# Kernel optimization log

Hardware: AMD Instinct MI355X
Metric: run time of the kernel (lower is better)

## Reference

```python
import jax, jax.numpy as jnp
import numpy as np

B, S, D = 2, 4096, 512
H, DQK, DV, W = 8, 64, 64, 32
ORDER = 6  # 2^(2*6)=4096 cells: 64x64 Hilbert grid covers max_seq_len=4096


def hilbert_d2xy(d, order):
    """Vectorized standard Hilbert curve d->(x,y) mapping on a 2^order grid."""
    x = jnp.zeros_like(d)
    y = jnp.zeros_like(d)
    t = d
    s = 1
    for _ in range(order):
        rx = (t // 2) & 1
        ry = (t ^ rx) & 1
        swap = ry == 0
        flip = swap & (rx == 1)
        xf = jnp.where(flip, s - 1 - x, x)
        yf = jnp.where(flip, s - 1 - y, y)
        x, y = jnp.where(swap, yf, xf), jnp.where(swap, xf, yf)
        x = x + s * rx
        y = y + s * ry
        t = t // 4
        s = s * 2
    return jnp.stack([x, y], axis=-1)


def neighbor_idx(seq_len, window):
    d = jnp.arange(seq_len, dtype=jnp.int32)
    coords = hilbert_d2xy(d, ORDER).astype(jnp.float32)  # (S, 2)
    diff = coords[:, None, :] - coords[None, :, :]
    dist = jnp.sqrt((diff ** 2).sum(-1))  # (S, S)
    _, idx = jax.lax.top_k(-dist, window)  # k smallest distances
    return idx.astype(jnp.int32)


def setup_inputs() -> dict:
    key = jax.random.key(0)
    k1, k2, k3, k4, k5 = jax.random.split(key, 5)
    sc = float(1.0 / np.sqrt(D))
    return {
        "x": jax.random.normal(k1, (B, S, D), jnp.float32),
        "W_q": jax.random.normal(k2, (H * DQK, D), jnp.float32) * sc,
        "W_k": jax.random.normal(k3, (H * DQK, D), jnp.float32) * sc,
        "W_v": jax.random.normal(k4, (H * DV, D), jnp.float32) * sc,
        "W_o": jax.random.normal(k5, (D, H * DV), jnp.float32) * sc,
        "neighbor_indices": neighbor_idx(S, W),
    }


def reference(x, W_q, W_k, W_v, W_o, neighbor_indices):
    b, s, _ = x.shape
    q = (x @ W_q.T).reshape(b, s, H, DQK).transpose(0, 2, 1, 3)  # (b,h,s,d)
    k = (x @ W_k.T).reshape(b, s, H, DQK).transpose(0, 2, 1, 3)
    v = (x @ W_v.T).reshape(b, s, H, DV).transpose(0, 2, 1, 3)
    kn = k[:, :, neighbor_indices, :]  # gather -> (b,h,s,w,d)
    vn = v[:, :, neighbor_indices, :]
    scale = float(1.0 / np.sqrt(DQK))
    scores = jnp.einsum('bhsd,bhswd->bhsw', q, kn) * scale
    attn = jax.nn.softmax(scores, axis=-1)
    out = jnp.einsum('bhsw,bhswd->bhsd', attn, vn)
    out = out.transpose(0, 2, 1, 3).reshape(b, s, H * DV)
    return out @ W_o.T
```

## Files before the change

### kernel.cpp

```cpp
#include <hip/hip_runtime.h>
#include <hip/hip_bf16.h>
#include <stdint.h>
#include <stddef.h>

constexpr int Bc = 2;
constexpr int Sc = 4096;
constexpr int Dc = 512;
constexpr int Hc = 8;
constexpr int Wc = 32;

using bf16_t = __bf16;
typedef __attribute__((ext_vector_type(8))) __bf16 bf16x8;
typedef __attribute__((ext_vector_type(4))) __bf16 bf16x4;
typedef __attribute__((ext_vector_type(2))) __bf16 bf16x2;
typedef __attribute__((ext_vector_type(4))) float f32x4;

__device__ __forceinline__ void async_copy16(const void* g, void* l) {
    __builtin_amdgcn_global_load_lds(
        (const __attribute__((address_space(1))) void*)g,
        (__attribute__((address_space(3))) void*)l,
        16, 0, 0);
}

__global__ void convert_all(const float* __restrict__ x,
                            const float* __restrict__ wq, const float* __restrict__ wk,
                            const float* __restrict__ wv, const float* __restrict__ wo,
                            bf16_t* __restrict__ xc, bf16_t* __restrict__ dq,
                            bf16_t* __restrict__ dk, bf16_t* __restrict__ dv,
                            bf16_t* __restrict__ dwo) {
    const int blk = blockIdx.x;
    const float* s; bf16_t* d; int base;
    if (blk < 4096) { s = x; d = xc; base = blk * 1024; }
    else {
        const int r = blk - 4096, which = r >> 8;
        s = (which == 0) ? wq : (which == 1) ? wk : (which == 2) ? wv : wo;
        d = (which == 0) ? dq : (which == 1) ? dk : (which == 2) ? dv : dwo;
        base = (r & 255) * 1024;
    }
    const int i = base + threadIdx.x * 4;
    const float4 v = *(const float4*)(s + i);
    bf16x4 o; o[0] = (bf16_t)v.x; o[1] = (bf16_t)v.y;
    o[2] = (bf16_t)v.z; o[3] = (bf16_t)v.w;
    *(bf16x4*)(d + i) = o;
}

template<int BM, int BN, int TM, int TN, bool F32OUT>
__global__ __launch_bounds__(256) void gemm_bt(
    const bf16_t* __restrict__ A, int lda,
    const bf16_t* __restrict__ B0, const bf16_t* __restrict__ B1,
    const bf16_t* __restrict__ B2, int ldb, int nPerB,
    void* __restrict__ C, int ldc, int K)
{
    constexpr int BK = 32;
    __shared__ __align__(1024) bf16_t Alds[BM * BK];
    __shared__ __align__(1024) bf16_t Blds[BN * BK];

    const int tid  = threadIdx.x;
    const int lane = tid & 63;
    const int wv   = tid >> 6;
    const int wm   = wv >> 1;
    const int wn   = wv & 1;
    const int r    = lane & 15;
    const int q4   = lane >> 4;

    const int blkM = blockIdx.x * BM;
    const int colC = blockIdx.y * BN;

    const bf16_t* Bp = B0;
    int nB = colC;
    if (nPerB > 0) {
        int wsel = colC / nPerB;
        nB = colC - wsel * nPerB;
        Bp = (wsel == 0) ? B0 : (wsel == 1) ? B1 : B2;
    }

    f32x4 acc[TM][TN];
    const f32x4 fzero = {0.f, 0.f, 0.f, 0.f};
    #pragma unroll
    for (int i = 0; i < TM; ++i)
        #pragma unroll
        for (int j = 0; j < TN; ++j) acc[i][j] = fzero;

    constexpr int A_LOADS = (BM * BK * 2) / (256 * 16);
    constexpr int B_LOADS = (BN * BK * 2) / (256 * 16);

    for (int kk = 0; kk < K; kk += BK) {
        __syncthreads();
        #pragma unroll
        for (int i = 0; i < A_LOADS; ++i) {
            int off  = i * 4096 + tid * 16;
            int row  = off >> 6;
            int colb = off & 63;
            const char* g = (const char*)A + ((size_t)(blkM + row) * lda + kk) * 2 + colb;
            async_copy16(g, (char*)Alds + off);
        }
        #pragma unroll
        for (int i = 0; i < B_LOADS; ++i) {
            int off  = i * 4096 + tid * 16;
            int row  = off >> 6;
            int colb = off & 63;
            const char* g = (const char*)Bp + ((size_t)(nB + row) * ldb + kk) * 2 + colb;
            async_copy16(g, (char*)Blds + off);
        }
        __syncthreads();

        bf16x8 af[TM], bfr[TN];
        #pragma unroll
        for (int mt = 0; mt < TM; ++mt)
            af[mt] = *(const bf16x8*)&Alds[(wm * TM * 16 + mt * 16 + r) * BK + q4 * 8];
        #pragma unroll
        for (int nt = 0; nt < TN; ++nt)
            bfr[nt] = *(const bf16x8*)&Blds[(wn * TN * 16 + nt * 16 + r) * BK + q4 * 8];

        #pragma unroll
        for (int mt = 0; mt < TM; ++mt)
            #pragma unroll
            for (int nt = 0; nt < TN; ++nt)
                acc[mt][nt] = __builtin_amdgcn_mfma_f32_16x16x32_bf16(
                    af[mt], bfr[nt], acc[mt][nt], 0, 0, 0);
    }

    #pragma unroll
    for (int mt = 0; mt < TM; ++mt) {
        #pragma unroll
        for (int nt = 0; nt < TN; ++nt) {
            int rr0 = blkM + wm * TM * 16 + mt * 16 + q4 * 4;
            int cc  = colC + wn * TN * 16 + nt * 16 + r;
            #pragma unroll
            for (int i = 0; i < 4; ++i) {
                size_t o = (size_t)(rr0 + i) * ldc + cc;
                if constexpr (F32OUT) ((float*)C)[o]  = acc[mt][nt][i];
                else                  ((bf16_t*)C)[o] = (bf16_t)acc[mt][nt][i];
            }
        }
    }
}

__global__ __launch_bounds__(256) void attn_fast(
    const bf16_t* __restrict__ QKV,
    const int*    __restrict__ nidx,
    bf16_t*       __restrict__ attn_out)
{
    const int lane = threadIdx.x & 63;
    const int wv   = threadIdx.x >> 6;

    const int bi  = blockIdx.x;
    const int blk = (bi & 7) * 2048 + (bi >> 3);
    const int wg  = blk * 4 + wv;
    const int s = wg & (Sc - 1);
    const int h = (wg >> 12) & (Hc - 1);
    const int b = wg >> 15;
    const size_t row = (size_t)b * Sc + s;

    const int d8 = lane & 7;
    const int wq = lane >> 3;

    const char* qkvB  = (const char*)QKV;
    const bf16x8 q8   = *(const bf16x8*)(qkvB + row * 3072 + h * 128 + d8 * 16);
    const char* Kbase = qkvB + (size_t)b * Sc * 3072 + 1024 + h * 128 + d8 * 16;
    const char* Vbase = qkvB + (size_t)b * Sc * 3072 + 2048 + h * 128 + d8 * 16;

    float  p[4];
    bf16x8 v8s[4];
    #pragma unroll
    for (int g = 0; g < 4; ++g) {
        const int t = nidx[s * Wc + g * 8 + wq];
        const size_t toff = (size_t)t * 3072;
        const bf16x8 k8 = *(const bf16x8*)(Kbase + toff);
        v8s[g] = *(const bf16x8*)(Vbase + toff);
        float d = 0.f;
        #pragma unroll
        for (int j = 0; j < 8; ++j) d += (float)q8[j] * (float)k8[j];
        d += __shfl_xor(d, 1);
        d += __shfl_xor(d, 2);
        d += __shfl_xor(d, 4);
        p[g] = d * 0.125f;
    }

    float mx = fmaxf(fmaxf(p[0], p[1]), fmaxf(p[2], p[3]));
    mx = fmaxf(mx, __shfl_xor(mx, 8));
    mx = fmaxf(mx, __shfl_xor(mx, 16));
    mx = fmaxf(mx, __shfl_xor(mx, 32));
    float e[4];
    float sum = 0.f;
    #pragma unroll
    for (int g = 0; g < 4; ++g) { e[g] = __expf(p[g] - mx); sum += e[g]; }
    sum += __shfl_xor(sum, 8);
    sum += __shfl_xor(sum, 16);
    sum += __shfl_xor(sum, 32);
    const float inv = 1.0f / sum;

    float acc[8] = {0.f, 0.f, 0.f, 0.f, 0.f, 0.f, 0.f, 0.f};
    #pragma unroll
    for (int g = 0; g < 4; ++g) {
        const float ag = e[g] * inv;
        #pragma unroll
        for (int j = 0; j < 8; ++j)
            acc[j] = fmaf(ag, (float)v8s[g][j], acc[j]);
    }
    #pragma unroll
    for (int j = 0; j < 8; ++j) {
        acc[j] += __shfl_xor(acc[j], 8);
        acc[j] += __shfl_xor(acc[j], 16);
        acc[j] += __shfl_xor(acc[j], 32);
    }
    if (wq == 0) {
        bf16x8 o;
        #pragma unroll
        for (int j = 0; j < 8; ++j) o[j] = (bf16_t)acc[j];
        *(bf16x8*)((char*)attn_out + row * 1024 + h * 128 + d8 * 16) = o;
    }
}

extern "C" void kernel_launch(void* const* d_in, const int* in_sizes, int n_in,
                              void* d_out, int out_size, void* d_ws, size_t ws_size,
                              hipStream_t stream) {
    (void)in_sizes; (void)n_in; (void)out_size; (void)ws_size;
    const int* nidx = (const int*)d_in[5];
    const int M = Bc * Sc;
    float* out = (float*)d_out;

    char* w = (char*)d_ws;
    bf16_t* xc   = (bf16_t*)(w + 256);
    bf16_t* Wqc  = xc  + 4194304;
    bf16_t* Wkc  = Wqc + 262144;
    bf16_t* Wvc  = Wkc + 262144;
    bf16_t* Woc  = Wvc + 262144;
    bf16_t* qkv  = Woc + 262144;
    bf16_t* attnS = xc;

    convert_all<<<5120, 256, 0, stream>>>(
        (const float*)d_in[0], (const float*)d_in[1], (const float*)d_in[2],
        (const float*)d_in[3], (const float*)d_in[4],
        xc, Wqc, Wkc, Wvc, Woc);

    gemm_bt<128, 128, 4, 4, false><<<dim3(M / 128, 1536 / 128), 256, 0, stream>>>(
        xc, Dc, Wqc, Wkc, Wvc, Dc, 512, qkv, 1536, Dc);

    attn_fast<<<(Bc * Hc * Sc) / 4, 256, 0, stream>>>(qkv, nidx, attnS);

    gemm_bt<128, 64, 4, 2, true><<<dim3(M / 128, 512 / 64), 256, 0, stream>>>(
        attnS, 512, Woc, Woc, Woc, 512, 0, out, Dc, Dc);
}
```

Before: 144.2 us.

## Replace QKV projection GEMM with 256x256-tile multi-stage pipelined kernel

Swaps the QKV projection GEMM for a dedicated kernel. It uses 256x256 tiles with 512 threads and a 4-deep LDS ring buffer filled by async global-to-LDS loads, gated by explicit vmcnt waits and barriers. Loads for later K-slices now overlap MFMA work on the current slice instead of syncing every iteration, and the wave priority is raised during the MFMA bursts. The cost is 128KB of LDS per block and only 192 blocks, so occupancy and CU coverage drop compared with the previous 768-block launch.

```diff
diff --git a/kernel.cpp b/kernel.cpp
--- a/kernel.cpp
+++ b/kernel.cpp
@@ -44,6 +44,112 @@
     *(bf16x4*)(d + i) = o;
 }
 
+__global__ __launch_bounds__(512, 2) void gemm8p(
+    const bf16_t* __restrict__ A,
+    const bf16_t* __restrict__ B0, const bf16_t* __restrict__ B1,
+    const bf16_t* __restrict__ B2,
+    bf16_t* __restrict__ C)
+{
+    __shared__ __align__(1024) char lds[131072];
+    char* ldsA = lds;
+    char* ldsB = lds + 65536;
+
+    const int tid  = threadIdx.x;
+    const int lane = tid & 63;
+    const int wv_  = tid >> 6;
+    const int wm   = wv_ >> 2;
+    const int wn   = wv_ & 3;
+    const int r    = lane & 15;
+    const int q4   = lane >> 4;
+
+    int id = blockIdx.y * gridDim.x + blockIdx.x;
+    id = (id & 7) * 24 + (id >> 3);
+    const int bxi = id & 31;
+    const int byi = id >> 5;
+    const int blkM = bxi * 256;
+    const int colC = byi * 256;
+
+    const int wsel = colC >> 9;
+    const int nB   = colC & 511;
+    const bf16_t* Bp = (wsel == 0) ? B0 : (wsel == 1) ? B1 : B2;
+
+    f32x4 acc[8][4];
+    const f32x4 fzero = {0.f, 0.f, 0.f, 0.f};
+    #pragma unroll
+    for (int i = 0; i < 8; ++i)
+        #pragma unroll
+        for (int j = 0; j < 4; ++j) acc[i][j] = fzero;
+
+    auto stage = [&](int h) {
+        const int kcol = h * 32;
+        char* dA = ldsA + ((h >> 1) & 1) * 32768 + (h & 1) * 16384;
+        char* dB = ldsB + ((h >> 1) & 1) * 32768 + (h & 1) * 16384;
+        #pragma unroll
+        for (int i = 0; i < 2; ++i) {
+            const int o = i * 8192 + tid * 16;
+            const int row = o >> 6, colb = o & 63;
+            async_copy16((const char*)A + ((size_t)(blkM + row) * 512 + kcol) * 2 + colb,
+                         dA + o);
+        }
+        #pragma unroll
+        for (int i = 0; i < 2; ++i) {
+            const int o = i * 8192 + tid * 16;
+            const int row = o >> 6, colb = o & 63;
+            async_copy16((const char*)Bp + ((size_t)(nB + row) * 512 + kcol) * 2 + colb,
+                         dB + o);
+        }
+    };
+
+    auto phase = [&](int p) {
+        const char* aB = ldsA + ((p >> 1) & 1) * 32768 + (p & 1) * 16384;
+        const char* bB = ldsB + ((p >> 1) & 1) * 32768 + (p & 1) * 16384;
+        bf16x8 af[8], bfr[4];
+        #pragma unroll
+        for (int mt = 0; mt < 8; ++mt)
+            af[mt] = *(const bf16x8*)(aB + (wm * 128 + mt * 16 + r) * 64 + q4 * 16);
+        #pragma unroll
+        for (int nt = 0; nt < 4; ++nt)
+            bfr[nt] = *(const bf16x8*)(bB + (wn * 64 + nt * 16 + r) * 64 + q4 * 16);
+        __builtin_amdgcn_s_setprio(1);
+        #pragma unroll
+        for (int mt = 0; mt < 8; ++mt)
+            #pragma unroll
+            for (int nt = 0; nt < 4; ++nt)
+                acc[mt][nt] = __builtin_amdgcn_mfma_f32_16x16x32_bf16(
+                    af[mt], bfr[nt], acc[mt][nt], 0, 0, 0);
+        __builtin_amdgcn_s_setprio(0);
+    };
+
+    stage(0); stage(1); stage(2);
+    asm volatile("s_waitcnt vmcnt(8)" ::: "memory");
+    __builtin_amdgcn_s_barrier();
+
+    for (int p = 0; p < 13; ++p) {
+        stage(p + 3);
+        phase(p);
+        asm volatile("s_waitcnt vmcnt(8)" ::: "memory");
+        __builtin_amdgcn_s_barrier();
+    }
+    phase(13);
+    asm volatile("s_waitcnt vmcnt(4)" ::: "memory");
+    __builtin_amdgcn_s_barrier();
+    phase(14);
+    asm volatile("s_waitcnt vmcnt(0)" ::: "memory");
+    __builtin_amdgcn_s_barrier();
+    phase(15);
+
+    #pragma unroll
+    for (int mt = 0; mt < 8; ++mt)
+        #pragma unroll
+        for (int nt = 0; nt < 4; ++nt) {
+            const int rr0 = blkM + wm * 128 + mt * 16 + q4 * 4;
+            const int cc  = colC + wn * 64 + nt * 16 + r;
+            #pragma unroll
+            for (int i = 0; i < 4; ++i)
+                C[(size_t)(rr0 + i) * 1536 + cc] = (bf16_t)acc[mt][nt][i];
+        }
+}
+
 template<int BM, int BN, int TM, int TN, bool F32OUT>
 __global__ __launch_bounds__(256) void gemm_bt(
     const bf16_t* __restrict__ A, int lda,
@@ -234,8 +340,7 @@
         (const float*)d_in[3], (const float*)d_in[4],
         xc, Wqc, Wkc, Wvc, Woc);
 
-    gemm_bt<128, 128, 4, 4, false><<<dim3(M / 128, 1536 / 128), 256, 0, stream>>>(
-        xc, Dc, Wqc, Wkc, Wvc, Dc, 512, qkv, 1536, Dc);
+    gemm8p<<<dim3(32, 6), 512, 0, stream>>>(xc, Wqc, Wkc, Wvc, qkv);
 
     attn_fast<<<(Bc * Hc * Sc) / 4, 256, 0, stream>>>(qkv, nidx, attnS);
 
```

After: 142.4 us. About the same (-1.2%).
